# Kernel optimization log

Measured on AMD Instinct MI355X. Metric: run time of the kernel, lower is better.

Reference implementation:

```python
import jax, jax.numpy as jnp
import numpy as np

TAU = 0.6      # critical_fractile from params()
GAMMA = 0.1    # L2-regularization weight (init arg)
N_ITERS = 60   # bisection iterations (machine precision on [0,1])
EPS = 1e-12

# The cvxpy problem per sample (prob vector p over support y):
#   min_z  p @ pinball(y - z) + GAMMA * ||p * (y - z)||_2,   0 <= z <= 1
# with pinball(e) = max(TAU*e, (TAU-1)*e). This is a 1-D convex problem in z;
# we solve the stationarity condition g(z) = df/dz = 0 by bisection (g is
# nondecreasing), then take one Newton step at the root so implicit gradients
# w.r.t. p flow correctly (dz/dp = -(dg/dp)/(dg/dz)). Fully batched over B.

def setup_inputs() -> dict:
    key = jax.random.key(0)
    B, S = 32768, 1001
    x = jax.random.uniform(key, (B, S), dtype=jnp.float32)
    x = x / x.sum(-1, keepdims=True)                      # probability vectors
    y_supp = jnp.linspace(0.0, 1.0, S, dtype=jnp.float32)  # support grid
    return {"x": x, "y_supp": y_supp}


def _grad_z(z, p, y):
    """g(z)=df/dz and its z-derivative, batched. z:[B], p:[B,S], y:[S]."""
    e = y[None, :] - z[:, None]                                  # [B,S]
    pin = jnp.sum(p * jnp.where(e >= 0, -TAU, 1.0 - TAU), -1)    # d(pinball)/dz
    pe = p * e
    nrm = jnp.sqrt(jnp.sum(pe * pe, -1) + EPS)                   # ||p*e||
    s1 = jnp.sum(p * p * e, -1)
    g = pin - GAMMA * s1 / nrm
    gp = GAMMA * (jnp.sum(p * p, -1) / nrm - (s1 * s1) / (nrm ** 3))
    return g, gp


def _solve(x, y):
    B = x.shape[0]
    p0 = jax.lax.stop_gradient(x)
    y0 = jax.lax.stop_gradient(y)
    lo = jnp.zeros((B,), x.dtype)
    hi = jnp.ones((B,), x.dtype)

    def body(carry, _):
        lo, hi = carry
        mid = 0.5 * (lo + hi)
        g, _ = _grad_z(mid, p0, y0)
        lo = jnp.where(g < 0, mid, lo)
        hi = jnp.where(g < 0, hi, mid)
        return (lo, hi), None

    (lo, hi), _ = jax.lax.scan(body, (lo, hi), None, length=N_ITERS)
    z0 = jax.lax.stop_gradient(0.5 * (lo + hi))
    # one Newton step at the root -> correct implicit gradients w.r.t. x, y
    g, gp = _grad_z(z0, x, y)
    z = z0 - g / jnp.maximum(gp, 1e-8)
    # boundary clamp (minimum at 0 or 1 if g doesn't change sign)
    g0, _ = _grad_z(jnp.zeros((B,), x.dtype), p0, y0)
    g1, _ = _grad_z(jnp.ones((B,), x.dtype), p0, y0)
    z = jnp.where(g0 >= 0, 0.0, jnp.where(g1 <= 0, 1.0, jnp.clip(z, 0.0, 1.0)))
    return z


def reference(x, y_supp):
    z = _solve(x, y_supp)                   # [B]
    e = y_supp[None, :] - z[:, None]        # error variable, [B,S]
    pinball = jnp.maximum(TAU * e, (TAU - 1.0) * e)  # pinball_loss at optimum
    w_error = x * e                          # w_error variable
    return (z[:, None], pinball, e, w_error)
```

## Files before the change

### kernel.cpp

```cpp
#include <hip/hip_runtime.h>
#include <hip/hip_bf16.h>


constexpr int NS   = 1001;
constexpr int SPAD = 1024;
constexpr int NT   = 256;

__global__ __launch_bounds__(NT) void newsvendor_kernel(
    const float* __restrict__ x,
    const float* __restrict__ ysup,
    float* __restrict__ out,
    int B)
{
    __shared__ float  sp[SPAD];
    __shared__ float  sy[SPAD];
    __shared__ double scdf[SPAD];
    __shared__ double wred[12];
    __shared__ double wtot[4];
    __shared__ int    wredi[4];
    __shared__ double bc[4];
    __shared__ float  zf_sh;

    const int row  = blockIdx.x;
    const int tid  = threadIdx.x;
    const int lane = tid & 63;
    const int wv   = tid >> 6;
    const float* xr = x + (size_t)row * NS;

    for (int i = tid; i < SPAD; i += NT) {
        sp[i] = (i < NS) ? xr[i]   : 0.0f;
        sy[i] = (i < NS) ? ysup[i] : 2.0f;
    }
    __syncthreads();

    double a = 0.0, b1 = 0.0, c2 = 0.0;
    for (int i = tid; i < NS; i += NT) {
        double p = (double)sp[i], y = (double)sy[i];
        double pp = p * p;
        a += pp; b1 += pp * y; c2 += pp * (y * y);
    }
    for (int off = 32; off > 0; off >>= 1) {
        a  += __shfl_xor(a,  off);
        b1 += __shfl_xor(b1, off);
        c2 += __shfl_xor(c2, off);
    }
    if (lane == 0) { wred[wv*3+0] = a; wred[wv*3+1] = b1; wred[wv*3+2] = c2; }

    const int base = tid * 4;
    double p0 = sp[base], p1 = sp[base+1], p2 = sp[base+2], p3 = sp[base+3];
    double l0 = 0.0, l1 = p0, l2 = p0+p1, l3 = p0+p1+p2;
    double s  = p0+p1+p2+p3;
    double inc = s;
    for (int d = 1; d < 64; d <<= 1) {
        double t = __shfl_up(inc, (unsigned)d);
        if (lane >= d) inc += t;
    }
    if (lane == 63) wtot[wv] = inc;
    __syncthreads();

    double woff = 0.0;
    for (int w = 0; w < wv; ++w) woff += wtot[w];
    double ebase = woff + (inc - s);
    scdf[base]   = ebase + l0;
    scdf[base+1] = ebase + l1;
    scdf[base+2] = ebase + l2;
    scdf[base+3] = ebase + l3;
    if (tid == 0) {
        bc[0] = wred[0]+wred[3]+wred[6]+wred[9];
        bc[1] = wred[1]+wred[4]+wred[7]+wred[10];
        bc[2] = wred[2]+wred[5]+wred[8]+wred[11];
    }
    __syncthreads();

    const double A   = bc[0], B1 = bc[1], C = bc[2];
    const double Pt  = scdf[NS];
    const double ca  = (double)0.6f;
    const double cb  = (double)0.4f;
    const double cab = ca + cb;
    const double GA  = (double)0.1f;
    const double EPSd = (double)1e-12f;

    int kmin = 0x7fffffff;
    for (int k = tid; k < NS; k += NT) {
        double z  = (double)sy[k];
        double s1 = B1 - z * A;
        double q  = C - z * (2.0 * B1 - z * A);
        double nr = sqrt(q + EPSd);
        double g  = cab * scdf[k] - ca * Pt - GA * s1 / nr;
        if (g >= 0.0) kmin = min(kmin, k);
    }
    for (int off = 32; off > 0; off >>= 1)
        kmin = min(kmin, __shfl_xor(kmin, off));
    if (lane == 0) wredi[wv] = kmin;
    __syncthreads();

    if (tid == 0) {
        int kstar = min(min(wredi[0], wredi[1]), min(wredi[2], wredi[3]));

        double g0 = -ca * Pt - GA * B1 / sqrt(C + EPSd);
        int c1 = (sy[NS-1] < 1.0f) ? NS : NS - 1;
        double s1b = B1 - A;
        double q1  = C - (2.0 * B1 - A);
        double g1 = cab * scdf[c1] - ca * Pt - GA * s1b / sqrt(q1 + EPSd);

        float zf;
        if (g0 >= 0.0)      zf = 0.0f;
        else if (g1 <= 0.0) zf = 1.0f;
        else {
            int kk = kstar;
            float zlF, zrF;
            if (kk >= NS) { kk = NS; zlF = sy[NS-1]; zrF = 1.0f; }
            else {
                zlF = (kk > 0) ? sy[kk-1] : 0.0f;
                zrF = sy[kk];
            }
            double Phat = cab * scdf[kk] - ca * Pt;

            auto Feval = [&](double z, double& gp) -> double {
                double s1 = B1 - z * A;
                double q  = C - z * (2.0 * B1 - z * A);
                double nr = sqrt(q + EPSd);
                gp = GA * (A / nr - (s1 * s1) / (nr * nr * nr));
                return Phat - GA * s1 / nr;
            };

            double dgp;
            double Fl = Feval((double)zlF, dgp);
            bool  jumpc;
            double zeta;
            if (Fl >= 0.0) { jumpc = true; zeta = (double)zlF; }
            else {
                jumpc = false;
                double lo = (double)zlF, hi = (double)zrF;
                double z = 0.5 * (lo + hi);
                for (int it = 0; it < 30; ++it) {
                    double gp; double F = Feval(z, gp);
                    if (F < 0.0) lo = z; else hi = z;
                    double zn = z - F / fmax(gp, 1e-300);
                    if (!(zn > lo && zn < hi)) zn = 0.5 * (lo + hi);
                    z = zn;
                }
                zeta = z;
            }

            float flo = 0.0f, fhi = 1.0f;
            for (int it = 0; it < 60; ++it) {
                float mid = 0.5f * (flo + fhi);
                bool dec = jumpc ? (mid <= zlF) : ((double)mid < zeta);
                if (dec) flo = mid; else fhi = mid;
            }
            float z0 = 0.5f * (flo + fhi);

            int cnt = (kk - 1) + ((zlF < z0) ? 1 : 0) + ((zrF < z0) ? 1 : 0);
            if (cnt < 0) cnt = 0;

            double z0d = (double)z0;
            double s1 = B1 - z0d * A;
            double q  = C - z0d * (2.0 * B1 - z0d * A);
            double nr = sqrt(q + EPSd);
            double g  = cab * scdf[cnt] - ca * Pt - GA * s1 / nr;
            double gp = GA * (A / nr - (s1 * s1) / (nr * nr * nr));
            double zn = z0d - g / fmax(gp, (double)1e-8f);
            zn = fmin(fmax(zn, 0.0), 1.0);
            zf = (float)zn;
        }
        zf_sh = zf;
    }
    __syncthreads();

    const float zf = zf_sh;
    const size_t Bz = (size_t)B;
    const size_t rb = (size_t)row * NS;
    float* outPin = out + Bz + rb;
    float* outE   = out + Bz + Bz * NS + rb;
    float* outW   = out + Bz + 2 * Bz * NS + rb;
    if (tid == 0) out[row] = zf;
    for (int i = tid; i < NS; i += NT) {
        float e  = sy[i] - zf;
        float pb = fmaxf(0.6f * e, -0.4f * e);
        outPin[i] = pb;
        outE[i]   = e;
        outW[i]   = sp[i] * e;
    }
}

extern "C" void kernel_launch(void* const* d_in, const int* in_sizes, int n_in,
                              void* d_out, int out_size, void* d_ws, size_t ws_size,
                              hipStream_t stream)
{
    const float* x = (const float*)d_in[0];
    const float* y = (const float*)d_in[1];
    float* out = (float*)d_out;
    const int Ssz = in_sizes[1];
    const int B   = in_sizes[0] / Ssz;
    newsvendor_kernel<<<B, NT, 0, stream>>>(x, y, out, B);
}
```

Baseline: 586.5 us.

## Replace sqrt/div sign tests and Newton root solve with closed-form algebra

```diff
diff --git a/kernel.cpp b/kernel.cpp
--- a/kernel.cpp
+++ b/kernel.cpp
@@ -72,22 +72,25 @@
     }
     __syncthreads();
 
-    const double A   = bc[0], B1 = bc[1], C = bc[2];
-    const double Pt  = scdf[NS];
-    const double ca  = (double)0.6f;
-    const double cb  = (double)0.4f;
-    const double cab = ca + cb;
-    const double GA  = (double)0.1f;
+    const double A    = bc[0], B1 = bc[1], C = bc[2];
+    const double Pt   = scdf[NS];
+    const double ca   = (double)0.6f;
+    const double cb   = (double)0.4f;
+    const double cab  = ca + cb;
+    const double GA   = (double)0.1f;
+    const double GA2  = GA * GA;
     const double EPSd = (double)1e-12f;
 
     int kmin = 0x7fffffff;
     for (int k = tid; k < NS; k += NT) {
         double z  = (double)sy[k];
+        double t  = cab * scdf[k] - ca * Pt;
         double s1 = B1 - z * A;
-        double q  = C - z * (2.0 * B1 - z * A);
-        double nr = sqrt(q + EPSd);
-        double g  = cab * scdf[k] - ca * Pt - GA * s1 / nr;
-        if (g >= 0.0) kmin = min(kmin, k);
+        double qe = C - z * (2.0 * B1 - z * A) + EPSd;
+        double lq = t * t * qe, rq = GA2 * s1 * s1;
+        bool ge = (t >= 0.0) ? (s1 <= 0.0 || lq >= rq)
+                             : (s1 <  0.0 && lq <= rq);
+        if (ge) kmin = min(kmin, k);
     }
     for (int off = 32; off > 0; off >>= 1)
         kmin = min(kmin, __shfl_xor(kmin, off));
@@ -100,8 +103,8 @@
         double g0 = -ca * Pt - GA * B1 / sqrt(C + EPSd);
         int c1 = (sy[NS-1] < 1.0f) ? NS : NS - 1;
         double s1b = B1 - A;
-        double q1  = C - (2.0 * B1 - A);
-        double g1 = cab * scdf[c1] - ca * Pt - GA * s1b / sqrt(q1 + EPSd);
+        double qe1 = C - (2.0 * B1 - A) + EPSd;
+        double g1 = cab * scdf[c1] - ca * Pt - GA * s1b / sqrt(qe1);
 
         float zf;
         if (g0 >= 0.0)      zf = 0.0f;
@@ -116,31 +119,23 @@
             }
             double Phat = cab * scdf[kk] - ca * Pt;
 
-            auto Feval = [&](double z, double& gp) -> double {
-                double s1 = B1 - z * A;
-                double q  = C - z * (2.0 * B1 - z * A);
-                double nr = sqrt(q + EPSd);
-                gp = GA * (A / nr - (s1 * s1) / (nr * nr * nr));
-                return Phat - GA * s1 / nr;
-            };
+            double zl  = (double)zlF;
+            double s1l = B1 - zl * A;
+            double qel = C - zl * (2.0 * B1 - zl * A) + EPSd;
+            double lql = Phat * Phat * qel, rql = GA2 * s1l * s1l;
+            bool Flge = (Phat >= 0.0) ? (s1l <= 0.0 || lql >= rql)
+                                      : (s1l <  0.0 && lql <= rql);
 
-            double dgp;
-            double Fl = Feval((double)zlF, dgp);
-            bool  jumpc;
+            bool   jumpc;
             double zeta;
-            if (Fl >= 0.0) { jumpc = true; zeta = (double)zlF; }
+            if (Flge) { jumpc = true; zeta = zl; }
             else {
                 jumpc = false;
-                double lo = (double)zlF, hi = (double)zrF;
-                double z = 0.5 * (lo + hi);
-                for (int it = 0; it < 30; ++it) {
-                    double gp; double F = Feval(z, gp);
-                    if (F < 0.0) lo = z; else hi = z;
-                    double zn = z - F / fmax(gp, 1e-300);
-                    if (!(zn > lo && zn < hi)) zn = 0.5 * (lo + hi);
-                    z = zn;
-                }
-                zeta = z;
+                double E  = (C * A - B1 * B1) + A * EPSd;
+                double cc = Phat / (GA * sqrt(A));
+                double u  = cc * sqrt(E / fmax(1.0 - cc * cc, 1e-300));
+                zeta = (B1 - u) / A;
+                zeta = fmin(fmax(zeta, zl), (double)zrF);
             }
 
             float flo = 0.0f, fhi = 1.0f;
@@ -156,10 +151,11 @@
 
             double z0d = (double)z0;
             double s1 = B1 - z0d * A;
-            double q  = C - z0d * (2.0 * B1 - z0d * A);
-            double nr = sqrt(q + EPSd);
-            double g  = cab * scdf[cnt] - ca * Pt - GA * s1 / nr;
-            double gp = GA * (A / nr - (s1 * s1) / (nr * nr * nr));
+            double qe = C - z0d * (2.0 * B1 - z0d * A) + EPSd;
+            double nr = sqrt(qe);
+            double inv = 1.0 / nr;
+            double g  = cab * scdf[cnt] - ca * Pt - GA * s1 * inv;
+            double gp = GA * inv * (A - s1 * s1 * (inv * inv));
             double zn = z0d - g / fmax(gp, (double)1e-8f);
             zn = fmin(fmax(zn, 0.0), 1.0);
             zf = (float)zn;
```

Result: faster. 551.4 us (-6.0%).
